# Performance work log

Hardware: AMD Instinct MI355X
Metric: run time of the kernel (lower is better)

Reference implementation:

```python
import jax, jax.numpy as jnp
import numpy as np

B, N, D = 4, 10000, 64
C, E = 2, 160000  # adj channels, edges per (graph, channel)
EPS = 1e-10


def setup_inputs() -> dict:
    key = jax.random.key(0)
    k1, k2, k3 = jax.random.split(key, 3)
    inputs = jax.random.normal(k1, (B, N, D), dtype=jnp.float32)
    edge_idx = jax.random.randint(k2, (B, C, E, 2), 0, N, dtype=jnp.int32)
    weight_a = 0.1 * jax.random.normal(k3, (C, 2 * D, 1), dtype=jnp.float32)
    return {"inputs": inputs, "edge_idx": edge_idx, "weight_a": weight_a}


def _gat_channel(x, idx, wa):
    # x: [N, D], idx: [E, 2] (col 0 = scatter/dst node, col 1 = gather/src node), wa: [2D, 1]
    n = x.shape[0]
    a1 = x[idx[:, 1]]                      # [E, D]
    a2 = x[idx[:, 0]]                      # [E, D]
    score = jnp.concatenate([a1, a2], axis=1) @ wa   # [E, 1]
    e = jnp.exp(jax.nn.leaky_relu(score, negative_slope=0.2))  # [E, 1]
    denom = jax.ops.segment_sum(e, idx[:, 0], num_segments=n)  # [N, 1]  (ii @ e)
    denom_e = denom[idx[:, 1]]             # [E, 1]  (faithful to original: gather by idx[:,1])
    alpha = e / (denom_e + EPS)            # [E, 1]
    r = jax.ops.segment_sum(alpha * a1, idx[:, 0], num_segments=n)  # [N, D]
    return jax.nn.sigmoid(r)


def _gat_graph(x, idx_all, weight_a):
    # x: [N, D], idx_all: [C, E, 2], weight_a: [C, 2D, 1]
    per_ch = jax.vmap(_gat_channel, in_axes=(None, 0, 0))(x, idx_all, weight_a)  # [C, N, D]
    return per_ch.sum(axis=0)


def reference(inputs, edge_idx, weight_a):
    # inputs: [B, N, D], edge_idx: [B, C, E, 2], weight_a: [C, 2D, 1]
    return jax.vmap(_gat_graph, in_axes=(0, 0, None))(inputs, edge_idx, weight_a)
```

## Files before the change

kernel.cpp:

```cpp
#include <hip/hip_runtime.h>

#define B_ 4
#define N_ 10000
#define D_ 64
#define C_ 2
#define E_ 160000
#define BC_ (B_ * C_)
#define SH2_ 7
#define NB2_ 128
#define G2_ 79
#define CAPF_ 2560
#define NBLK_ 125
#define EPT_ 5
#define EPB_ (256 * EPT_)
#define YBLK_ (BC_ * 40)
#define EPS_ 1e-10f

__global__ void gat_yb(const float* __restrict__ x, const float* __restrict__ wa,
                       float* __restrict__ y1, float* __restrict__ y0,
                       const int* __restrict__ eidx, int* __restrict__ gcount,
                       unsigned int* __restrict__ bpack) {
    int tid = threadIdx.x;
    if (blockIdx.x < YBLK_) {
        int bc = blockIdx.x & 7;
        int n  = (blockIdx.x >> 3) * 256 + tid;
        if (n >= N_) return;
        int b = bc / C_, c = bc % C_;
        const float4* xr = (const float4*)(x + ((size_t)b * N_ + n) * D_);
        const float4* w1 = (const float4*)(wa + (size_t)c * 2 * D_);
        const float4* w0 = w1 + D_ / 4;
        float a = 0.f, bb = 0.f;
#pragma unroll
        for (int i = 0; i < D_ / 4; ++i) {
            float4 xv = xr[i];
            float4 u = w1[i], v = w0[i];
            a  += xv.x * u.x + xv.y * u.y + xv.z * u.z + xv.w * u.w;
            bb += xv.x * v.x + xv.y * v.y + xv.z * v.z + xv.w * v.w;
        }
        y1[bc * N_ + n] = a;
        y0[bc * N_ + n] = bb;
        return;
    }
    int bid = blockIdx.x - YBLK_;
    int bc  = bid & 7;
    int blk = bid >> 3;
    const int2* ep = (const int2*)eidx + (size_t)bc * E_ + (size_t)blk * EPB_;
    __shared__ int sd[128];
    __shared__ int excl[G2_], cur[G2_], gbase[G2_];
    __shared__ unsigned int stage[EPB_];
    if (tid < 128) sd[tid] = 0;
    __syncthreads();
    unsigned int pk[EPT_];
    int gg[EPT_];
#pragma unroll
    for (int k = 0; k < EPT_; ++k) {
        int2 v = ep[k * 256 + tid];
        int g  = v.x >> SH2_;
        gg[k]  = g;
        pk[k]  = ((unsigned int)g << 21) |
                 ((unsigned int)(v.x & (NB2_ - 1)) << 14) |
                 (unsigned int)v.y;
        atomicAdd(&sd[g], 1);
    }
    __syncthreads();
    int cnt = (tid < 128) ? sd[tid] : 0;
    for (int off = 1; off < 128; off <<= 1) {
        int t = (tid < 128 && tid >= off) ? sd[tid - off] : 0;
        __syncthreads();
        if (tid < 128) sd[tid] += t;
        __syncthreads();
    }
    if (tid < G2_) {
        int ex = sd[tid] - cnt;
        excl[tid]  = ex;
        cur[tid]   = ex;
        gbase[tid] = atomicAdd(&gcount[bc * G2_ + tid], cnt);
    }
    __syncthreads();
#pragma unroll
    for (int k = 0; k < EPT_; ++k) {
        int slot = atomicAdd(&cur[gg[k]], 1);
        stage[slot] = pk[k];
    }
    __syncthreads();
#pragma unroll
    for (int k = 0; k < EPT_; ++k) {
        int idx = k * 256 + tid;
        unsigned int p = stage[idx];
        int g     = p >> 21;
        int local = idx - excl[g];
        bpack[((size_t)bc * G2_ + g) * CAPF_ + gbase[g] + local] =
            (((p >> 14) & 127u) << 16) | (p & 16383u);
    }
}

__global__ void gat_fine(const unsigned int* __restrict__ bpack,
                         const int* __restrict__ gcount,
                         const float* __restrict__ y1, const float* __restrict__ y0,
                         unsigned short* __restrict__ csr_i1, float* __restrict__ csr_ee,
                         int* __restrict__ rs_s, int* __restrict__ rs_e,
                         float* __restrict__ rd) {
    int bc = blockIdx.x & 7;
    int g  = blockIdx.x >> 3;
    int K  = gcount[bc * G2_ + g];
    int R  = (bc * G2_ + g) * CAPF_;
    const unsigned int* bp = bpack + R;
    const float* y1p = y1 + bc * N_;
    int tid = threadIdx.x;

    __shared__ int   cnt[NB2_], excl[NB2_], cur[NB2_], sd[NB2_];
    __shared__ float y0l[NB2_];
    __shared__ unsigned short li1[CAPF_];
    __shared__ float lee[CAPF_];

    int node = g * NB2_ + tid;
    if (tid < NB2_) {
        cnt[tid] = 0;
        y0l[tid] = (node < N_) ? y0[bc * N_ + node] : 0.f;
    }
    __syncthreads();

    for (int j = tid; j < K; j += 256)
        atomicAdd(&cnt[bp[j] >> 16], 1);
    __syncthreads();

    int v = 0;
    if (tid < NB2_) { v = cnt[tid]; sd[tid] = v; }
    __syncthreads();
    for (int off = 1; off < NB2_; off <<= 1) {
        int t = (tid < NB2_ && tid >= off) ? sd[tid - off] : 0;
        __syncthreads();
        if (tid < NB2_) sd[tid] += t;
        __syncthreads();
    }
    if (tid < NB2_) {
        int ex = sd[tid] - v;
        excl[tid] = ex;
        cur[tid]  = ex;
        if (node < N_) {
            rs_s[bc * N_ + node] = R + ex;
            rs_e[bc * N_ + node] = R + ex + v;
        }
    }
    __syncthreads();

    for (int j = tid; j < K; j += 256) {
        unsigned int p = bp[j];
        int ln = p >> 16;
        int i1 = p & 0xffff;
        int slot = atomicAdd(&cur[ln], 1);
        li1[slot] = (unsigned short)i1;
        float sc = y1p[i1] + y0l[ln];
        lee[slot] = __expf(sc > 0.f ? sc : 0.2f * sc);
    }
    __syncthreads();

    if (tid < NB2_ && node < N_) {
        int s = excl[tid], t = s + v;
        float sum = 0.f;
        for (int j = s; j < t; ++j) sum += lee[j];
        rd[bc * N_ + node] = 1.f / (sum + EPS_);
    }
    for (int j = tid; j < K; j += 256) {
        csr_i1[R + j] = li1[j];
        csr_ee[R + j] = lee[j];
    }
}

__global__ void gat_acc(const float* __restrict__ x, const int* __restrict__ rs_s,
                        const int* __restrict__ rs_e,
                        const unsigned short* __restrict__ csr_i1,
                        const float* __restrict__ csr_ee, const float* __restrict__ rd,
                        float* __restrict__ out) {
    int lane = threadIdx.x & 63;
    int w    = threadIdx.x >> 6;
    int b    = blockIdx.x & 3;
    int nn   = blockIdx.x >> 2;
    int n    = nn * 2 + (w >> 1);
    int c    = w & 1;
    int bc = b * C_ + c;
    const float* xb  = x + (size_t)b * N_ * D_ + lane;
    const float* rdp = rd + bc * N_;
    int s = rs_s[bc * N_ + n], t = rs_e[bc * N_ + n];
    float acc = 0.f;
    for (int base = s; base < t; base += 64) {
        int m = t - base; if (m > 64) m = 64;
        int a = 0; float wgt = 0.f;
        if (lane < m) {
            a   = csr_i1[base + lane];
            wgt = csr_ee[base + lane] * rdp[a];
        }
        int mp = (m + 7) & ~7;
        for (int j = 0; j < mp; j += 8) {
            int   a0 = __shfl(a, j),     a1 = __shfl(a, j + 1);
            int   a2 = __shfl(a, j + 2), a3 = __shfl(a, j + 3);
            int   a4 = __shfl(a, j + 4), a5 = __shfl(a, j + 5);
            int   a6 = __shfl(a, j + 6), a7 = __shfl(a, j + 7);
            float w0 = __shfl(wgt, j),     w1 = __shfl(wgt, j + 1);
            float w2 = __shfl(wgt, j + 2), w3 = __shfl(wgt, j + 3);
            float w4 = __shfl(wgt, j + 4), w5 = __shfl(wgt, j + 5);
            float w6 = __shfl(wgt, j + 6), w7 = __shfl(wgt, j + 7);
            float x0 = xb[a0 * D_], x1 = xb[a1 * D_];
            float x2 = xb[a2 * D_], x3 = xb[a3 * D_];
            float x4 = xb[a4 * D_], x5 = xb[a5 * D_];
            float x6 = xb[a6 * D_], x7 = xb[a7 * D_];
            acc += w0 * x0;
            acc += w1 * x1;
            acc += w2 * x2;
            acc += w3 * x3;
            acc += w4 * x4;
            acc += w5 * x5;
            acc += w6 * x6;
            acc += w7 * x7;
        }
    }
    float sg = 1.f / (1.f + __expf(-acc));
    __shared__ float sh[2][64];
    if (c == 1) sh[w >> 1][lane] = sg;
    __syncthreads();
    if (c == 0) out[((size_t)b * N_ + n) * D_ + lane] = sg + sh[w >> 1][lane];
}

extern "C" void kernel_launch(void* const* d_in, const int* in_sizes, int n_in,
                              void* d_out, int out_size, void* d_ws, size_t ws_size,
                              hipStream_t stream) {
    const float* x    = (const float*)d_in[0];
    const int*   eidx = (const int*)d_in[1];
    const float* wa   = (const float*)d_in[2];
    float* out = (float*)d_out;

    int*   gcount = (int*)d_ws;
    float* y1     = (float*)d_ws + 1024;
    float* y0     = y1 + BC_ * N_;
    float* rd     = y0 + BC_ * N_;
    int*   rs_s   = (int*)(rd + BC_ * N_);
    int*   rs_e   = rs_s + BC_ * N_;
    unsigned int* bpack  = (unsigned int*)(rs_e + BC_ * N_);
    float*        csr_ee = (float*)(bpack + (size_t)BC_ * G2_ * CAPF_);
    unsigned short* csr_i1 = (unsigned short*)(csr_ee + (size_t)BC_ * G2_ * CAPF_);

    hipMemsetAsync(gcount, 0, BC_ * G2_ * sizeof(int), stream);

    gat_yb  <<<YBLK_ + BC_ * NBLK_, 256, 0, stream>>>(x, wa, y1, y0, eidx, gcount, bpack);
    gat_fine<<<BC_ * G2_,           256, 0, stream>>>(bpack, gcount, y1, y0,
                                                      csr_i1, csr_ee, rs_s, rs_e, rd);
    gat_acc <<<B_ * N_ / 2,         256, 0, stream>>>(x, rs_s, rs_e, csr_i1, csr_ee, rd, out);
}
```

Before: 133.1 us.

## Recompute edge exp in accumulate kernel instead of storing per-edge scores

The fine kernel now computes per-node denominators with shared float atomics during the counting pass and no longer writes per-edge exp values to global memory. It emits a packed (y1, reciprocal denominator) pair per node. The accumulate kernel recomputes each edge's exp from that pair and y0, and broadcasts index and weight through shared memory instead of shuffles. This removes the csr_ee write and read traffic and one gather, at the cost of redundant exp work and float atomics in LDS, whose summation order is nondeterministic.

New measurement: 129.3 us. 1.03x faster.

```diff
diff --git a/kernel.cpp b/kernel.cpp
--- a/kernel.cpp
+++ b/kernel.cpp
@@ -97,9 +97,9 @@
 __global__ void gat_fine(const unsigned int* __restrict__ bpack,
                          const int* __restrict__ gcount,
                          const float* __restrict__ y1, const float* __restrict__ y0,
-                         unsigned short* __restrict__ csr_i1, float* __restrict__ csr_ee,
+                         unsigned short* __restrict__ csr_i1,
                          int* __restrict__ rs_s, int* __restrict__ rs_e,
-                         float* __restrict__ rd) {
+                         float2* __restrict__ yrd) {
     int bc = blockIdx.x & 7;
     int g  = blockIdx.x >> 3;
     int K  = gcount[bc * G2_ + g];
@@ -109,19 +109,26 @@
     int tid = threadIdx.x;
 
     __shared__ int   cnt[NB2_], excl[NB2_], cur[NB2_], sd[NB2_];
-    __shared__ float y0l[NB2_];
+    __shared__ float y0l[NB2_], den[NB2_];
     __shared__ unsigned short li1[CAPF_];
-    __shared__ float lee[CAPF_];
 
     int node = g * NB2_ + tid;
     if (tid < NB2_) {
         cnt[tid] = 0;
+        den[tid] = 0.f;
         y0l[tid] = (node < N_) ? y0[bc * N_ + node] : 0.f;
     }
     __syncthreads();
 
-    for (int j = tid; j < K; j += 256)
-        atomicAdd(&cnt[bp[j] >> 16], 1);
+    for (int j = tid; j < K; j += 256) {
+        unsigned int p = bp[j];
+        int ln = p >> 16;
+        int i1 = p & 0xffff;
+        float sc = y1p[i1] + y0l[ln];
+        float ev = __expf(sc > 0.f ? sc : 0.2f * sc);
+        atomicAdd(&cnt[ln], 1);
+        atomicAdd(&den[ln], ev);
+    }
     __syncthreads();
 
     int v = 0;
@@ -140,37 +147,26 @@
         if (node < N_) {
             rs_s[bc * N_ + node] = R + ex;
             rs_e[bc * N_ + node] = R + ex + v;
+            yrd[bc * N_ + node]  = make_float2(y1p[node], 1.f / (den[tid] + EPS_));
         }
     }
     __syncthreads();
 
     for (int j = tid; j < K; j += 256) {
         unsigned int p = bp[j];
-        int ln = p >> 16;
-        int i1 = p & 0xffff;
-        int slot = atomicAdd(&cur[ln], 1);
-        li1[slot] = (unsigned short)i1;
-        float sc = y1p[i1] + y0l[ln];
-        lee[slot] = __expf(sc > 0.f ? sc : 0.2f * sc);
-    }
-    __syncthreads();
-
-    if (tid < NB2_ && node < N_) {
-        int s = excl[tid], t = s + v;
-        float sum = 0.f;
-        for (int j = s; j < t; ++j) sum += lee[j];
-        rd[bc * N_ + node] = 1.f / (sum + EPS_);
-    }
-    for (int j = tid; j < K; j += 256) {
+        int slot = atomicAdd(&cur[p >> 16], 1);
+        li1[slot] = (unsigned short)(p & 0xffff);
+    }
+    __syncthreads();
+
+    for (int j = tid; j < K; j += 256)
         csr_i1[R + j] = li1[j];
-        csr_ee[R + j] = lee[j];
-    }
 }
 
 __global__ void gat_acc(const float* __restrict__ x, const int* __restrict__ rs_s,
                         const int* __restrict__ rs_e,
                         const unsigned short* __restrict__ csr_i1,
-                        const float* __restrict__ csr_ee, const float* __restrict__ rd,
+                        const float2* __restrict__ yrd, const float* __restrict__ y0,
                         float* __restrict__ out) {
     int lane = threadIdx.x & 63;
     int w    = threadIdx.x >> 6;
@@ -179,39 +175,40 @@
     int n    = nn * 2 + (w >> 1);
     int c    = w & 1;
     int bc = b * C_ + c;
-    const float* xb  = x + (size_t)b * N_ * D_ + lane;
-    const float* rdp = rd + bc * N_;
+    const float* xb = x + (size_t)b * N_ * D_ + lane;
+    const float2* yrdp = yrd + bc * N_;
     int s = rs_s[bc * N_ + n], t = rs_e[bc * N_ + n];
+    float y0n = y0[bc * N_ + n];
+    __shared__ float2 meta[4][64];
     float acc = 0.f;
     for (int base = s; base < t; base += 64) {
         int m = t - base; if (m > 64) m = 64;
         int a = 0; float wgt = 0.f;
         if (lane < m) {
-            a   = csr_i1[base + lane];
-            wgt = csr_ee[base + lane] * rdp[a];
-        }
+            a = csr_i1[base + lane];
+            float2 yr = yrdp[a];
+            float sc = yr.x + y0n;
+            wgt = __expf(sc > 0.f ? sc : 0.2f * sc) * yr.y;
+        }
+        meta[w][lane] = make_float2(__int_as_float(a), wgt);
         int mp = (m + 7) & ~7;
         for (int j = 0; j < mp; j += 8) {
-            int   a0 = __shfl(a, j),     a1 = __shfl(a, j + 1);
-            int   a2 = __shfl(a, j + 2), a3 = __shfl(a, j + 3);
-            int   a4 = __shfl(a, j + 4), a5 = __shfl(a, j + 5);
-            int   a6 = __shfl(a, j + 6), a7 = __shfl(a, j + 7);
-            float w0 = __shfl(wgt, j),     w1 = __shfl(wgt, j + 1);
-            float w2 = __shfl(wgt, j + 2), w3 = __shfl(wgt, j + 3);
-            float w4 = __shfl(wgt, j + 4), w5 = __shfl(wgt, j + 5);
-            float w6 = __shfl(wgt, j + 6), w7 = __shfl(wgt, j + 7);
-            float x0 = xb[a0 * D_], x1 = xb[a1 * D_];
-            float x2 = xb[a2 * D_], x3 = xb[a3 * D_];
-            float x4 = xb[a4 * D_], x5 = xb[a5 * D_];
-            float x6 = xb[a6 * D_], x7 = xb[a7 * D_];
-            acc += w0 * x0;
-            acc += w1 * x1;
-            acc += w2 * x2;
-            acc += w3 * x3;
-            acc += w4 * x4;
-            acc += w5 * x5;
-            acc += w6 * x6;
-            acc += w7 * x7;
+            float2 m0 = meta[w][j],     m1 = meta[w][j + 1];
+            float2 m2 = meta[w][j + 2], m3 = meta[w][j + 3];
+            float2 m4 = meta[w][j + 4], m5 = meta[w][j + 5];
+            float2 m6 = meta[w][j + 6], m7 = meta[w][j + 7];
+            float x0 = xb[__float_as_int(m0.x) * D_], x1 = xb[__float_as_int(m1.x) * D_];
+            float x2 = xb[__float_as_int(m2.x) * D_], x3 = xb[__float_as_int(m3.x) * D_];
+            float x4 = xb[__float_as_int(m4.x) * D_], x5 = xb[__float_as_int(m5.x) * D_];
+            float x6 = xb[__float_as_int(m6.x) * D_], x7 = xb[__float_as_int(m7.x) * D_];
+            acc += m0.y * x0;
+            acc += m1.y * x1;
+            acc += m2.y * x2;
+            acc += m3.y * x3;
+            acc += m4.y * x4;
+            acc += m5.y * x5;
+            acc += m6.y * x6;
+            acc += m7.y * x7;
         }
     }
     float sg = 1.f / (1.f + __expf(-acc));
@@ -229,20 +226,19 @@
     const float* wa   = (const float*)d_in[2];
     float* out = (float*)d_out;
 
-    int*   gcount = (int*)d_ws;
-    float* y1     = (float*)d_ws + 1024;
-    float* y0     = y1 + BC_ * N_;
-    float* rd     = y0 + BC_ * N_;
-    int*   rs_s   = (int*)(rd + BC_ * N_);
-    int*   rs_e   = rs_s + BC_ * N_;
-    unsigned int* bpack  = (unsigned int*)(rs_e + BC_ * N_);
-    float*        csr_ee = (float*)(bpack + (size_t)BC_ * G2_ * CAPF_);
-    unsigned short* csr_i1 = (unsigned short*)(csr_ee + (size_t)BC_ * G2_ * CAPF_);
+    int*    gcount = (int*)d_ws;
+    float*  y1     = (float*)d_ws + 1024;
+    float*  y0     = y1 + BC_ * N_;
+    float2* yrd    = (float2*)(y0 + BC_ * N_);
+    int*    rs_s   = (int*)(yrd + BC_ * N_);
+    int*    rs_e   = rs_s + BC_ * N_;
+    unsigned int* bpack = (unsigned int*)(rs_e + BC_ * N_);
+    unsigned short* csr_i1 = (unsigned short*)(bpack + (size_t)BC_ * G2_ * CAPF_);
 
     hipMemsetAsync(gcount, 0, BC_ * G2_ * sizeof(int), stream);
 
     gat_yb  <<<YBLK_ + BC_ * NBLK_, 256, 0, stream>>>(x, wa, y1, y0, eidx, gcount, bpack);
     gat_fine<<<BC_ * G2_,           256, 0, stream>>>(bpack, gcount, y1, y0,
-                                                      csr_i1, csr_ee, rs_s, rs_e, rd);
-    gat_acc <<<B_ * N_ / 2,         256, 0, stream>>>(x, rs_s, rs_e, csr_i1, csr_ee, rd, out);
-}
+                                                      csr_i1, rs_s, rs_e, yrd);
+    gat_acc <<<B_ * N_ / 2,         256, 0, stream>>>(x, rs_s, rs_e, csr_i1, yrd, y0, out);
+}
```
